# Kernel optimization log

Hardware: AMD Instinct MI355X
Metric: run time of the kernel (lower is better)

Reference implementation:

```python
import jax, jax.numpy as jnp
import numpy as np

N_NODES = 50000
N_EDGES = 800000
IN_F = 128
HID = 128
OUT_F = 128
NUM_LAYERS = 3


def _glorot(key, shape):
    fan_in, fan_out = shape
    lim = np.sqrt(6.0 / (fan_in + fan_out)).astype(np.float32)
    return jax.random.uniform(key, shape, jnp.float32, -lim, lim)


def setup_inputs() -> dict:
    key = jax.random.key(0)
    ks = jax.random.split(key, 12)
    x = jax.random.normal(ks[0], (N_NODES, IN_F), jnp.float32)
    edge_index = jax.random.randint(ks[1], (2, N_EDGES), 0, N_NODES, jnp.int64)
    dims = [(IN_F, HID), (HID, HID), (HID, OUT_F)]
    inp = {"x": x, "edge_index": edge_index}
    for i, (di, do) in enumerate(dims):
        inp[f"Wl{i}"] = _glorot(ks[2 + 3 * i], (di, do))      # neighbor (lin_l) weight
        inp[f"bl{i}"] = jnp.zeros((do,), jnp.float32)          # lin_l bias
        inp[f"Wr{i}"] = _glorot(ks[3 + 3 * i], (di, do))      # root (lin_r) weight, no bias
    return inp


def _sage_layer(x, src, dst, Wl, bl, Wr):
    # scatter-mean of source features onto destination nodes
    msg = x[src]                                               # [E, F] gather
    summed = jax.ops.segment_sum(msg, dst, num_segments=N_NODES)
    cnt = jax.ops.segment_sum(jnp.ones((src.shape[0],), x.dtype), dst,
                              num_segments=N_NODES)
    agg = summed / jnp.maximum(cnt, 1.0)[:, None]              # mean; 0 if no neighbors
    return agg @ Wl + bl + x @ Wr


def reference(x, edge_index, Wl0, bl0, Wr0, Wl1, bl1, Wr1, Wl2, bl2, Wr2):
    src, dst = edge_index[0], edge_index[1]
    params = [(Wl0, bl0, Wr0), (Wl1, bl1, Wr1), (Wl2, bl2, Wr2)]
    for i, (Wl, bl, Wr) in enumerate(params):
        x = _sage_layer(x, src, dst, Wl, bl, Wr)
        if i < NUM_LAYERS - 1:
            x = jax.nn.relu(x)
    return x
```

## Files before the change

kernel.cpp:

```cpp
#include <hip/hip_runtime.h>

#define F 128

typedef __attribute__((ext_vector_type(8))) short short8v;
typedef __attribute__((ext_vector_type(4))) float f32x4;

__device__ __forceinline__ unsigned short f2bf(float f) {
    unsigned int u = __builtin_bit_cast(unsigned int, f);
    unsigned int r = (u + 0x7fffu + ((u >> 16) & 1u)) >> 16;
    return (unsigned short)r;
}
__device__ __forceinline__ float bf2f(unsigned int b16) {
    unsigned int u = b16 << 16;
    return __builtin_bit_cast(float, u);
}

__device__ __forceinline__ int load_src(const int* ei, int is64, int E, int e) {
    return is64 ? ei[2 * e] : ei[e];
}
__device__ __forceinline__ int load_dst(const int* ei, int is64, int E, int e) {
    return is64 ? ei[2 * (E + e)] : ei[E + e];
}

__global__ void prep(const int* __restrict__ ei, int* __restrict__ flag,
                     int* __restrict__ deg, int N,
                     const float* __restrict__ x, unsigned short* __restrict__ xb,
                     int ndegb, int nxb,
                     const float* __restrict__ Wl0, const float* __restrict__ Wr0,
                     const float* __restrict__ Wl1, const float* __restrict__ Wr1,
                     const float* __restrict__ Wl2, const float* __restrict__ Wr2,
                     unsigned short* __restrict__ Wp) {
    int b = blockIdx.x;
    if (b < ndegb) {
        int i = b * 256 + threadIdx.x;
        if (i < N) deg[i] = 0;
        if (b == 0) {
            __shared__ int any_nonzero;
            if (threadIdx.x == 0) any_nonzero = 0;
            __syncthreads();
            int v = ei[2 * threadIdx.x + 1];
            if (v != 0) atomicOr(&any_nonzero, 1);
            __syncthreads();
            if (threadIdx.x == 0) *flag = (any_nonzero == 0) ? 1 : 0;
        }
        return;
    }
    if (b < ndegb + nxb) {
        int i = (b - ndegb) * 256 + threadIdx.x;
        float4 v = *(const float4*)(x + (size_t)i * 4);
        ushort4 o;
        o.x = f2bf(v.x); o.y = f2bf(v.y); o.z = f2bf(v.z); o.w = f2bf(v.w);
        *(ushort4*)(xb + (size_t)i * 4) = o;
        return;
    }
    int t = (b - ndegb - nxb) * 256 + threadIdx.x;
    int L = t >> 12;
    int tt = t & 4095;
    const float* Wl = (L == 0) ? Wl0 : (L == 1) ? Wl1 : Wl2;
    const float* Wr = (L == 0) ? Wr0 : (L == 1) ? Wr1 : Wr2;
    int lane = tt & 63;
    int nt = (tt >> 6) & 7;
    int kt = (tt >> 9) & 7;
    int c = nt * 16 + (lane & 15);
    int kbase = kt * 32 + ((lane >> 4) << 3);
    unsigned short o[8];
#pragma unroll
    for (int i = 0; i < 8; ++i) {
        int k = kbase + i;
        float v = (k < 128) ? Wl[k * F + c] : Wr[(k - 128) * F + c];
        o[i] = f2bf(v);
    }
    *(uint4*)(Wp + ((size_t)L * 32768) + (size_t)tt * 8) = *(const uint4*)o;
}

__global__ void count_rank(const int* __restrict__ ei, const int* __restrict__ flag,
                           int* __restrict__ deg, int* __restrict__ rank, int E) {
    int e = blockIdx.x * blockDim.x + threadIdx.x;
    if (e >= E) return;
    int is64 = *flag;
    int d = load_dst(ei, is64, E, e);
    rank[e] = atomicAdd(&deg[d], 1);
}

__global__ __launch_bounds__(1024) void scan_local(const int* __restrict__ deg,
                                                   int* __restrict__ rs,
                                                   int* __restrict__ partials, int N) {
    __shared__ int wsum[16];
    const int tid = threadIdx.x;
    const int lane = tid & 63, wid = tid >> 6;
    int i = blockIdx.x * 1024 + tid;
    int v = (i < N) ? deg[i] : 0;
    int incl = v;
#pragma unroll
    for (int d = 1; d < 64; d <<= 1) {
        int t = __shfl_up(incl, d);
        if (lane >= d) incl += t;
    }
    if (lane == 63) wsum[wid] = incl;
    __syncthreads();
    if (tid == 0) {
        int acc = 0;
#pragma unroll
        for (int w = 0; w < 16; ++w) { int t = wsum[w]; wsum[w] = acc; acc += t; }
        partials[blockIdx.x] = acc;
    }
    __syncthreads();
    if (i < N) rs[i] = wsum[wid] + (incl - v);
}

__global__ void scan_part(const int* __restrict__ partials, int* __restrict__ coff,
                          int nch) {
    int tid = threadIdx.x;
    int v = (tid < nch) ? partials[tid] : 0;
    int incl = v;
#pragma unroll
    for (int d = 1; d < 64; d <<= 1) {
        int t = __shfl_up(incl, d);
        if (tid >= d) incl += t;
    }
    coff[tid] = incl - v;
}

__global__ void fill_adj(const int* __restrict__ ei, const int* __restrict__ flag,
                         const int* __restrict__ rs, const int* __restrict__ coff,
                         const int* __restrict__ rank, int* __restrict__ adj, int E) {
    int e = blockIdx.x * blockDim.x + threadIdx.x;
    if (e >= E) return;
    int is64 = *flag;
    int s = load_src(ei, is64, E, e);
    int d = load_dst(ei, is64, E, e);
    adj[rs[d] + coff[d >> 10] + rank[e]] = s;
}

__global__ __launch_bounds__(256) void gather_mean(
    const unsigned short* __restrict__ xb, const int* __restrict__ adj,
    const int* __restrict__ rs, const int* __restrict__ coff,
    const int* __restrict__ deg, unsigned short* __restrict__ aggb, int N) {
    int n = (blockIdx.x * blockDim.x + threadIdx.x) >> 6;
    if (n >= N) return;
    const int lane = threadIdx.x & 63;
    const int q = lane >> 4, l4 = lane & 15;
    const int start = rs[n] + coff[n >> 10];
    const int d = deg[n];
    const unsigned short* xbase = xb + l4 * 8;
    float a0 = 0.f, a1 = 0.f, a2 = 0.f, a3 = 0.f;
    float a4 = 0.f, a5 = 0.f, a6 = 0.f, a7 = 0.f;
    int i = q;
    for (; i + 12 < d; i += 16) {
        int s0 = adj[start + i];
        int s1 = adj[start + i + 4];
        int s2 = adj[start + i + 8];
        int s3 = adj[start + i + 12];
        uint4 v0 = *(const uint4*)(xbase + (size_t)s0 * F);
        uint4 v1 = *(const uint4*)(xbase + (size_t)s1 * F);
        uint4 v2 = *(const uint4*)(xbase + (size_t)s2 * F);
        uint4 v3 = *(const uint4*)(xbase + (size_t)s3 * F);
        a0 += bf2f(v0.x & 0xffff) + bf2f(v1.x & 0xffff) + bf2f(v2.x & 0xffff) + bf2f(v3.x & 0xffff);
        a1 += bf2f(v0.x >> 16) + bf2f(v1.x >> 16) + bf2f(v2.x >> 16) + bf2f(v3.x >> 16);
        a2 += bf2f(v0.y & 0xffff) + bf2f(v1.y & 0xffff) + bf2f(v2.y & 0xffff) + bf2f(v3.y & 0xffff);
        a3 += bf2f(v0.y >> 16) + bf2f(v1.y >> 16) + bf2f(v2.y >> 16) + bf2f(v3.y >> 16);
        a4 += bf2f(v0.z & 0xffff) + bf2f(v1.z & 0xffff) + bf2f(v2.z & 0xffff) + bf2f(v3.z & 0xffff);
        a5 += bf2f(v0.z >> 16) + bf2f(v1.z >> 16) + bf2f(v2.z >> 16) + bf2f(v3.z >> 16);
        a6 += bf2f(v0.w & 0xffff) + bf2f(v1.w & 0xffff) + bf2f(v2.w & 0xffff) + bf2f(v3.w & 0xffff);
        a7 += bf2f(v0.w >> 16) + bf2f(v1.w >> 16) + bf2f(v2.w >> 16) + bf2f(v3.w >> 16);
    }
    for (; i < d; i += 4) {
        int s = adj[start + i];
        uint4 v = *(const uint4*)(xbase + (size_t)s * F);
        a0 += bf2f(v.x & 0xffff);
        a1 += bf2f(v.x >> 16);
        a2 += bf2f(v.y & 0xffff);
        a3 += bf2f(v.y >> 16);
        a4 += bf2f(v.z & 0xffff);
        a5 += bf2f(v.z >> 16);
        a6 += bf2f(v.w & 0xffff);
        a7 += bf2f(v.w >> 16);
    }
    a0 += __shfl_xor(a0, 16); a0 += __shfl_xor(a0, 32);
    a1 += __shfl_xor(a1, 16); a1 += __shfl_xor(a1, 32);
    a2 += __shfl_xor(a2, 16); a2 += __shfl_xor(a2, 32);
    a3 += __shfl_xor(a3, 16); a3 += __shfl_xor(a3, 32);
    a4 += __shfl_xor(a4, 16); a4 += __shfl_xor(a4, 32);
    a5 += __shfl_xor(a5, 16); a5 += __shfl_xor(a5, 32);
    a6 += __shfl_xor(a6, 16); a6 += __shfl_xor(a6, 32);
    a7 += __shfl_xor(a7, 16); a7 += __shfl_xor(a7, 32);
    if (q == 0) {
        float inv = 1.0f / fmaxf((float)d, 1.0f);
        uint4 o;
        o.x = ((unsigned int)f2bf(a1 * inv) << 16) | f2bf(a0 * inv);
        o.y = ((unsigned int)f2bf(a3 * inv) << 16) | f2bf(a2 * inv);
        o.z = ((unsigned int)f2bf(a5 * inv) << 16) | f2bf(a4 * inv);
        o.w = ((unsigned int)f2bf(a7 * inv) << 16) | f2bf(a6 * inv);
        *(uint4*)(aggb + (size_t)n * F + l4 * 8) = o;
    }
}

__global__ __launch_bounds__(512) void sage_mfma(
    const unsigned short* __restrict__ aggb, const unsigned short* __restrict__ xb,
    const unsigned short* __restrict__ Wpack, const float* __restrict__ bl,
    unsigned short* __restrict__ outb, float* __restrict__ outf,
    int N, int final_layer) {
    __shared__ unsigned short sW[32768];

    const int wid = threadIdx.x >> 6;
    const int lane = threadIdx.x & 63;
    const int row0 = (blockIdx.x * 8 + wid) * 16;
    const bool active = (row0 < N);

    short8v a[8];
    if (active) {
        const int rA = row0 + (lane & 15);
        const int kidx = (lane >> 4) << 3;
        const unsigned short* arow_a = aggb + (size_t)rA * F + kidx;
        const unsigned short* arow_x = xb + (size_t)rA * F + kidx;
#pragma unroll
        for (int kt = 0; kt < 4; ++kt) a[kt] = *(const short8v*)(arow_a + kt * 32);
#pragma unroll
        for (int kt = 4; kt < 8; ++kt) a[kt] = *(const short8v*)(arow_x + (kt - 4) * 32);
    }

    {
        const uint4* srcv = (const uint4*)Wpack;
        uint4* dstv = (uint4*)sW;
#pragma unroll
        for (int t = 0; t < 8; ++t)
            dstv[threadIdx.x + t * 512] = srcv[threadIdx.x + t * 512];
    }
    __syncthreads();
    if (!active) return;

    f32x4 acc[8];
#pragma unroll
    for (int nt = 0; nt < 8; ++nt) acc[nt] = (f32x4){0.f, 0.f, 0.f, 0.f};

#pragma unroll
    for (int kt = 0; kt < 8; ++kt) {
#pragma unroll
        for (int nt = 0; nt < 8; ++nt) {
            short8v b = *(const short8v*)(sW + ((kt * 8 + nt) * 64 + lane) * 8);
            acc[nt] = __builtin_amdgcn_mfma_f32_16x16x32_bf16(a[kt], b, acc[nt], 0, 0, 0);
        }
    }

    const int c0 = lane & 15;
    const int r0 = row0 + ((lane >> 4) << 2);
#pragma unroll
    for (int nt = 0; nt < 8; ++nt) {
        const int col = nt * 16 + c0;
        const float b = bl[col];
#pragma unroll
        for (int reg = 0; reg < 4; ++reg) {
            const int r = r0 + reg;
            float v = acc[nt][reg] + b;
            if (!final_layer) {
                v = fmaxf(v, 0.f);
                outb[(size_t)r * F + col] = f2bf(v);
            } else {
                outf[(size_t)r * F + col] = v;
            }
        }
    }
}

extern "C" void kernel_launch(void* const* d_in, const int* in_sizes, int n_in,
                              void* d_out, int out_size, void* d_ws, size_t ws_size,
                              hipStream_t stream) {
    const float* x = (const float*)d_in[0];
    const int* ei = (const int*)d_in[1];
    const int E = in_sizes[1] / 2;
    const int N = in_sizes[0] / F;
    const int NCH = (N + 1023) / 1024;

    const float* Wl[3] = {(const float*)d_in[2], (const float*)d_in[5], (const float*)d_in[8]};
    const float* bl[3] = {(const float*)d_in[3], (const float*)d_in[6], (const float*)d_in[9]};
    const float* Wr[3] = {(const float*)d_in[4], (const float*)d_in[7], (const float*)d_in[10]};
    float* out = (float*)d_out;

    char* ws = (char*)d_ws;
    size_t off = 0;
    auto alloc = [&](size_t bytes) {
        size_t o = off;
        off = (off + bytes + 255) & ~(size_t)255;
        return o;
    };
    int* flag = (int*)(ws + alloc(4));
    int* deg = (int*)(ws + alloc((size_t)N * 4));
    int* rs = (int*)(ws + alloc((size_t)N * 4));
    int* partials = (int*)(ws + alloc(64 * 4));
    int* coff = (int*)(ws + alloc(64 * 4));
    int* rank = (int*)(ws + alloc((size_t)E * 4));
    int* adj = (int*)(ws + alloc((size_t)E * 4));
    unsigned short* xb = (unsigned short*)(ws + alloc((size_t)N * F * 2));
    unsigned short* aggb = (unsigned short*)(ws + alloc((size_t)N * F * 2));
    unsigned short* h1b = (unsigned short*)(ws + alloc((size_t)N * F * 2));
    unsigned short* h2b = (unsigned short*)(ws + alloc((size_t)N * F * 2));
    unsigned short* Wp = (unsigned short*)(ws + alloc((size_t)3 * 4096 * 8 * 2));

    int ndegb = (N + 255) / 256;
    int nxb = (N * F / 4 + 255) / 256;
    prep<<<ndegb + nxb + 48, 256, 0, stream>>>(ei, flag, deg, N, x, xb, ndegb, nxb,
                                               Wl[0], Wr[0], Wl[1], Wr[1], Wl[2], Wr[2], Wp);

    count_rank<<<(E + 255) / 256, 256, 0, stream>>>(ei, flag, deg, rank, E);
    scan_local<<<NCH, 1024, 0, stream>>>(deg, rs, partials, N);
    scan_part<<<1, 64, 0, stream>>>(partials, coff, NCH);
    fill_adj<<<(E + 255) / 256, 256, 0, stream>>>(ei, flag, rs, coff, rank, adj, E);

    const unsigned short* cur = xb;
    unsigned short* hb[3] = {h1b, h2b, nullptr};
    int nwaves = (N + 15) / 16;
    int nblocks_m = (nwaves + 7) / 8;
    for (int layer = 0; layer < 3; ++layer) {
        gather_mean<<<(N * 64 + 255) / 256, 256, 0, stream>>>(cur, adj, rs, coff, deg, aggb, N);
        sage_mfma<<<nblocks_m, 512, 0, stream>>>(aggb, cur, Wp + (size_t)layer * 32768,
                                                 bl[layer], hb[layer], out, N, layer == 2);
        cur = hb[layer];
    }
}
```

Baseline: 191.2 us.

## Fuse neighbor mean-aggregation into MFMA layer kernel and fold chunk scan into consumers

Merges gather_mean and sage_mfma into one kernel. Each 512-thread block aggregates 128 nodes into a padded shared-memory tile, then runs the MFMA linear layer reading the aggregate from LDS and the weights straight from global memory. Each block of fill_adj and the fused kernel now recomputes the chunk-offset prefix scan itself, so the scan_part launch is gone. This removes the aggb global round trip and one launch per layer. In exchange, weights are no longer staged in shared memory, and each wave aggregates its 16 nodes serially, which may lower memory-level parallelism in the gather phase.

```diff
diff --git a/kernel.cpp b/kernel.cpp
--- a/kernel.cpp
+++ b/kernel.cpp
@@ -108,126 +108,128 @@
     if (i < N) rs[i] = wsum[wid] + (incl - v);
 }
 
-__global__ void scan_part(const int* __restrict__ partials, int* __restrict__ coff,
-                          int nch) {
-    int tid = threadIdx.x;
-    int v = (tid < nch) ? partials[tid] : 0;
-    int incl = v;
-#pragma unroll
-    for (int d = 1; d < 64; d <<= 1) {
-        int t = __shfl_up(incl, d);
-        if (tid >= d) incl += t;
-    }
-    coff[tid] = incl - v;
-}
-
 __global__ void fill_adj(const int* __restrict__ ei, const int* __restrict__ flag,
-                         const int* __restrict__ rs, const int* __restrict__ coff,
-                         const int* __restrict__ rank, int* __restrict__ adj, int E) {
+                         const int* __restrict__ rs, const int* __restrict__ partials,
+                         int nch, const int* __restrict__ rank,
+                         int* __restrict__ adj, int E) {
+    __shared__ int sCoff[64];
+    if (threadIdx.x < 64) {
+        int t = threadIdx.x;
+        int v = (t < nch) ? partials[t] : 0;
+        int incl = v;
+#pragma unroll
+        for (int d = 1; d < 64; d <<= 1) {
+            int s = __shfl_up(incl, d);
+            if (t >= d) incl += s;
+        }
+        sCoff[t] = incl - v;
+    }
+    __syncthreads();
     int e = blockIdx.x * blockDim.x + threadIdx.x;
     if (e >= E) return;
     int is64 = *flag;
     int s = load_src(ei, is64, E, e);
     int d = load_dst(ei, is64, E, e);
-    adj[rs[d] + coff[d >> 10] + rank[e]] = s;
-}
-
-__global__ __launch_bounds__(256) void gather_mean(
+    adj[rs[d] + sCoff[d >> 10] + rank[e]] = s;
+}
+
+#define AGG_PAD 136
+__global__ __launch_bounds__(512, 4) void sage_fused(
     const unsigned short* __restrict__ xb, const int* __restrict__ adj,
-    const int* __restrict__ rs, const int* __restrict__ coff,
-    const int* __restrict__ deg, unsigned short* __restrict__ aggb, int N) {
-    int n = (blockIdx.x * blockDim.x + threadIdx.x) >> 6;
-    if (n >= N) return;
-    const int lane = threadIdx.x & 63;
-    const int q = lane >> 4, l4 = lane & 15;
-    const int start = rs[n] + coff[n >> 10];
-    const int d = deg[n];
-    const unsigned short* xbase = xb + l4 * 8;
-    float a0 = 0.f, a1 = 0.f, a2 = 0.f, a3 = 0.f;
-    float a4 = 0.f, a5 = 0.f, a6 = 0.f, a7 = 0.f;
-    int i = q;
-    for (; i + 12 < d; i += 16) {
-        int s0 = adj[start + i];
-        int s1 = adj[start + i + 4];
-        int s2 = adj[start + i + 8];
-        int s3 = adj[start + i + 12];
-        uint4 v0 = *(const uint4*)(xbase + (size_t)s0 * F);
-        uint4 v1 = *(const uint4*)(xbase + (size_t)s1 * F);
-        uint4 v2 = *(const uint4*)(xbase + (size_t)s2 * F);
-        uint4 v3 = *(const uint4*)(xbase + (size_t)s3 * F);
-        a0 += bf2f(v0.x & 0xffff) + bf2f(v1.x & 0xffff) + bf2f(v2.x & 0xffff) + bf2f(v3.x & 0xffff);
-        a1 += bf2f(v0.x >> 16) + bf2f(v1.x >> 16) + bf2f(v2.x >> 16) + bf2f(v3.x >> 16);
-        a2 += bf2f(v0.y & 0xffff) + bf2f(v1.y & 0xffff) + bf2f(v2.y & 0xffff) + bf2f(v3.y & 0xffff);
-        a3 += bf2f(v0.y >> 16) + bf2f(v1.y >> 16) + bf2f(v2.y >> 16) + bf2f(v3.y >> 16);
-        a4 += bf2f(v0.z & 0xffff) + bf2f(v1.z & 0xffff) + bf2f(v2.z & 0xffff) + bf2f(v3.z & 0xffff);
-        a5 += bf2f(v0.z >> 16) + bf2f(v1.z >> 16) + bf2f(v2.z >> 16) + bf2f(v3.z >> 16);
-        a6 += bf2f(v0.w & 0xffff) + bf2f(v1.w & 0xffff) + bf2f(v2.w & 0xffff) + bf2f(v3.w & 0xffff);
-        a7 += bf2f(v0.w >> 16) + bf2f(v1.w >> 16) + bf2f(v2.w >> 16) + bf2f(v3.w >> 16);
-    }
-    for (; i < d; i += 4) {
-        int s = adj[start + i];
-        uint4 v = *(const uint4*)(xbase + (size_t)s * F);
-        a0 += bf2f(v.x & 0xffff);
-        a1 += bf2f(v.x >> 16);
-        a2 += bf2f(v.y & 0xffff);
-        a3 += bf2f(v.y >> 16);
-        a4 += bf2f(v.z & 0xffff);
-        a5 += bf2f(v.z >> 16);
-        a6 += bf2f(v.w & 0xffff);
-        a7 += bf2f(v.w >> 16);
-    }
-    a0 += __shfl_xor(a0, 16); a0 += __shfl_xor(a0, 32);
-    a1 += __shfl_xor(a1, 16); a1 += __shfl_xor(a1, 32);
-    a2 += __shfl_xor(a2, 16); a2 += __shfl_xor(a2, 32);
-    a3 += __shfl_xor(a3, 16); a3 += __shfl_xor(a3, 32);
-    a4 += __shfl_xor(a4, 16); a4 += __shfl_xor(a4, 32);
-    a5 += __shfl_xor(a5, 16); a5 += __shfl_xor(a5, 32);
-    a6 += __shfl_xor(a6, 16); a6 += __shfl_xor(a6, 32);
-    a7 += __shfl_xor(a7, 16); a7 += __shfl_xor(a7, 32);
-    if (q == 0) {
-        float inv = 1.0f / fmaxf((float)d, 1.0f);
-        uint4 o;
-        o.x = ((unsigned int)f2bf(a1 * inv) << 16) | f2bf(a0 * inv);
-        o.y = ((unsigned int)f2bf(a3 * inv) << 16) | f2bf(a2 * inv);
-        o.z = ((unsigned int)f2bf(a5 * inv) << 16) | f2bf(a4 * inv);
-        o.w = ((unsigned int)f2bf(a7 * inv) << 16) | f2bf(a6 * inv);
-        *(uint4*)(aggb + (size_t)n * F + l4 * 8) = o;
-    }
-}
-
-__global__ __launch_bounds__(512) void sage_mfma(
-    const unsigned short* __restrict__ aggb, const unsigned short* __restrict__ xb,
+    const int* __restrict__ rs, const int* __restrict__ partials, int nch,
+    const int* __restrict__ deg,
     const unsigned short* __restrict__ Wpack, const float* __restrict__ bl,
     unsigned short* __restrict__ outb, float* __restrict__ outf,
     int N, int final_layer) {
-    __shared__ unsigned short sW[32768];
+    __shared__ int sCoff[64];
+    __shared__ unsigned short sAgg[128][AGG_PAD];
 
     const int wid = threadIdx.x >> 6;
     const int lane = threadIdx.x & 63;
-    const int row0 = (blockIdx.x * 8 + wid) * 16;
-    const bool active = (row0 < N);
-
-    short8v a[8];
-    if (active) {
-        const int rA = row0 + (lane & 15);
-        const int kidx = (lane >> 4) << 3;
-        const unsigned short* arow_a = aggb + (size_t)rA * F + kidx;
-        const unsigned short* arow_x = xb + (size_t)rA * F + kidx;
-#pragma unroll
-        for (int kt = 0; kt < 4; ++kt) a[kt] = *(const short8v*)(arow_a + kt * 32);
-#pragma unroll
-        for (int kt = 4; kt < 8; ++kt) a[kt] = *(const short8v*)(arow_x + (kt - 4) * 32);
-    }
-
-    {
-        const uint4* srcv = (const uint4*)Wpack;
-        uint4* dstv = (uint4*)sW;
-#pragma unroll
-        for (int t = 0; t < 8; ++t)
-            dstv[threadIdx.x + t * 512] = srcv[threadIdx.x + t * 512];
-    }
-    __syncthreads();
-    if (!active) return;
+    const int row0 = blockIdx.x * 128;
+
+    if (wid == 0) {
+        int t = lane;
+        int v = (t < nch) ? partials[t] : 0;
+        int incl = v;
+#pragma unroll
+        for (int d = 1; d < 64; d <<= 1) {
+            int s = __shfl_up(incl, d);
+            if (t >= d) incl += s;
+        }
+        sCoff[t] = incl - v;
+    }
+    __syncthreads();
+
+    const int q = lane >> 4, l4 = lane & 15;
+    const unsigned short* xbase = xb + l4 * 8;
+    for (int r = 0; r < 16; ++r) {
+        const int lr = wid * 16 + r;
+        const int n = row0 + lr;
+        if (n >= N) break;
+        const int start = rs[n] + sCoff[n >> 10];
+        const int d = deg[n];
+        float a0 = 0.f, a1 = 0.f, a2 = 0.f, a3 = 0.f;
+        float a4 = 0.f, a5 = 0.f, a6 = 0.f, a7 = 0.f;
+        int i = q;
+        for (; i + 12 < d; i += 16) {
+            int s0 = adj[start + i];
+            int s1 = adj[start + i + 4];
+            int s2 = adj[start + i + 8];
+            int s3 = adj[start + i + 12];
+            uint4 v0 = *(const uint4*)(xbase + (size_t)s0 * F);
+            uint4 v1 = *(const uint4*)(xbase + (size_t)s1 * F);
+            uint4 v2 = *(const uint4*)(xbase + (size_t)s2 * F);
+            uint4 v3 = *(const uint4*)(xbase + (size_t)s3 * F);
+            a0 += bf2f(v0.x & 0xffff) + bf2f(v1.x & 0xffff) + bf2f(v2.x & 0xffff) + bf2f(v3.x & 0xffff);
+            a1 += bf2f(v0.x >> 16) + bf2f(v1.x >> 16) + bf2f(v2.x >> 16) + bf2f(v3.x >> 16);
+            a2 += bf2f(v0.y & 0xffff) + bf2f(v1.y & 0xffff) + bf2f(v2.y & 0xffff) + bf2f(v3.y & 0xffff);
+            a3 += bf2f(v0.y >> 16) + bf2f(v1.y >> 16) + bf2f(v2.y >> 16) + bf2f(v3.y >> 16);
+            a4 += bf2f(v0.z & 0xffff) + bf2f(v1.z & 0xffff) + bf2f(v2.z & 0xffff) + bf2f(v3.z & 0xffff);
+            a5 += bf2f(v0.z >> 16) + bf2f(v1.z >> 16) + bf2f(v2.z >> 16) + bf2f(v3.z >> 16);
+            a6 += bf2f(v0.w & 0xffff) + bf2f(v1.w & 0xffff) + bf2f(v2.w & 0xffff) + bf2f(v3.w & 0xffff);
+            a7 += bf2f(v0.w >> 16) + bf2f(v1.w >> 16) + bf2f(v2.w >> 16) + bf2f(v3.w >> 16);
+        }
+        for (; i < d; i += 4) {
+            int s = adj[start + i];
+            uint4 v = *(const uint4*)(xbase + (size_t)s * F);
+            a0 += bf2f(v.x & 0xffff);
+            a1 += bf2f(v.x >> 16);
+            a2 += bf2f(v.y & 0xffff);
+            a3 += bf2f(v.y >> 16);
+            a4 += bf2f(v.z & 0xffff);
+            a5 += bf2f(v.z >> 16);
+            a6 += bf2f(v.w & 0xffff);
+            a7 += bf2f(v.w >> 16);
+        }
+        a0 += __shfl_xor(a0, 16); a0 += __shfl_xor(a0, 32);
+        a1 += __shfl_xor(a1, 16); a1 += __shfl_xor(a1, 32);
+        a2 += __shfl_xor(a2, 16); a2 += __shfl_xor(a2, 32);
+        a3 += __shfl_xor(a3, 16); a3 += __shfl_xor(a3, 32);
+        a4 += __shfl_xor(a4, 16); a4 += __shfl_xor(a4, 32);
+        a5 += __shfl_xor(a5, 16); a5 += __shfl_xor(a5, 32);
+        a6 += __shfl_xor(a6, 16); a6 += __shfl_xor(a6, 32);
+        a7 += __shfl_xor(a7, 16); a7 += __shfl_xor(a7, 32);
+        if (q == 0) {
+            float inv = 1.0f / fmaxf((float)d, 1.0f);
+            uint4 o;
+            o.x = ((unsigned int)f2bf(a1 * inv) << 16) | f2bf(a0 * inv);
+            o.y = ((unsigned int)f2bf(a3 * inv) << 16) | f2bf(a2 * inv);
+            o.z = ((unsigned int)f2bf(a5 * inv) << 16) | f2bf(a4 * inv);
+            o.w = ((unsigned int)f2bf(a7 * inv) << 16) | f2bf(a6 * inv);
+            *(uint4*)&sAgg[lr][l4 * 8] = o;
+        }
+    }
+    __syncthreads();
+
+    const int row0w = row0 + wid * 16;
+    if (row0w >= N) return;
+
+    const int lrA = wid * 16 + (lane & 15);
+    const int kidx = (lane >> 4) << 3;
+    int rX = row0w + (lane & 15);
+    if (rX >= N) rX = N - 1;
+    const unsigned short* arow_x = xb + (size_t)rX * F + kidx;
 
     f32x4 acc[8];
 #pragma unroll
@@ -235,15 +237,18 @@
 
 #pragma unroll
     for (int kt = 0; kt < 8; ++kt) {
+        short8v a;
+        if (kt < 4) a = *(const short8v*)&sAgg[lrA][kt * 32 + kidx];
+        else        a = *(const short8v*)(arow_x + (kt - 4) * 32);
 #pragma unroll
         for (int nt = 0; nt < 8; ++nt) {
-            short8v b = *(const short8v*)(sW + ((kt * 8 + nt) * 64 + lane) * 8);
-            acc[nt] = __builtin_amdgcn_mfma_f32_16x16x32_bf16(a[kt], b, acc[nt], 0, 0, 0);
+            short8v b = *(const short8v*)(Wpack + ((size_t)(kt * 8 + nt) * 64 + lane) * 8);
+            acc[nt] = __builtin_amdgcn_mfma_f32_16x16x32_bf16(a, b, acc[nt], 0, 0, 0);
         }
     }
 
     const int c0 = lane & 15;
-    const int r0 = row0 + ((lane >> 4) << 2);
+    const int r0 = row0w + ((lane >> 4) << 2);
 #pragma unroll
     for (int nt = 0; nt < 8; ++nt) {
         const int col = nt * 16 + c0;
@@ -251,12 +256,14 @@
 #pragma unroll
         for (int reg = 0; reg < 4; ++reg) {
             const int r = r0 + reg;
-            float v = acc[nt][reg] + b;
-            if (!final_layer) {
-                v = fmaxf(v, 0.f);
-                outb[(size_t)r * F + col] = f2bf(v);
-            } else {
-                outf[(size_t)r * F + col] = v;
+            if (r < N) {
+                float v = acc[nt][reg] + b;
+                if (!final_layer) {
+                    v = fmaxf(v, 0.f);
+                    outb[(size_t)r * F + col] = f2bf(v);
+                } else {
+                    outf[(size_t)r * F + col] = v;
+                }
             }
         }
     }
@@ -287,11 +294,9 @@
     int* deg = (int*)(ws + alloc((size_t)N * 4));
     int* rs = (int*)(ws + alloc((size_t)N * 4));
     int* partials = (int*)(ws + alloc(64 * 4));
-    int* coff = (int*)(ws + alloc(64 * 4));
     int* rank = (int*)(ws + alloc((size_t)E * 4));
     int* adj = (int*)(ws + alloc((size_t)E * 4));
     unsigned short* xb = (unsigned short*)(ws + alloc((size_t)N * F * 2));
-    unsigned short* aggb = (unsigned short*)(ws + alloc((size_t)N * F * 2));
     unsigned short* h1b = (unsigned short*)(ws + alloc((size_t)N * F * 2));
     unsigned short* h2b = (unsigned short*)(ws + alloc((size_t)N * F * 2));
     unsigned short* Wp = (unsigned short*)(ws + alloc((size_t)3 * 4096 * 8 * 2));
@@ -303,17 +308,15 @@
 
     count_rank<<<(E + 255) / 256, 256, 0, stream>>>(ei, flag, deg, rank, E);
     scan_local<<<NCH, 1024, 0, stream>>>(deg, rs, partials, N);
-    scan_part<<<1, 64, 0, stream>>>(partials, coff, NCH);
-    fill_adj<<<(E + 255) / 256, 256, 0, stream>>>(ei, flag, rs, coff, rank, adj, E);
+    fill_adj<<<(E + 255) / 256, 256, 0, stream>>>(ei, flag, rs, partials, NCH, rank, adj, E);
 
     const unsigned short* cur = xb;
     unsigned short* hb[3] = {h1b, h2b, nullptr};
-    int nwaves = (N + 15) / 16;
-    int nblocks_m = (nwaves + 7) / 8;
+    int nblocks = (N + 127) / 128;
     for (int layer = 0; layer < 3; ++layer) {
-        gather_mean<<<(N * 64 + 255) / 256, 256, 0, stream>>>(cur, adj, rs, coff, deg, aggb, N);
-        sage_mfma<<<nblocks_m, 512, 0, stream>>>(aggb, cur, Wp + (size_t)layer * 32768,
-                                                 bl[layer], hb[layer], out, N, layer == 2);
+        sage_fused<<<nblocks, 512, 0, stream>>>(cur, adj, rs, partials, NCH, deg,
+                                                Wp + (size_t)layer * 32768, bl[layer],
+                                                hb[layer], out, N, layer == 2);
         cur = hb[layer];
     }
 }
```

Measured after the change: 260.4 us. +36.2%, slower.
